# Kernel tuning notes

Hardware: AMD Instinct MI355X
Metric: run time of the kernel (lower is better)

Reference implementation:

```python
import jax, jax.numpy as jnp
import numpy as np

N, M, H, C = 20000, 20000, 32, 128
KP_EXTENT = 0.6
EPS = 1e-5


def _kpconv(q_pts, s_pts, neighb_inds, x, kernel_points, weights):
    """Rigid KPConv, linear influence, 'sum' aggregation, Predator-style density norm."""
    # shadow point / shadow feature padding (index M is the shadow slot)
    s_pad = jnp.concatenate([s_pts, jnp.full((1, 3), 1e6, s_pts.dtype)], axis=0)
    x_pad = jnp.concatenate([x, jnp.zeros((1, x.shape[1]), x.dtype)], axis=0)
    neighbors = s_pad[neighb_inds] - q_pts[:, None, :]              # [N,H,3]
    diff = neighbors[:, :, None, :] - kernel_points[None, None]      # [N,H,K,3]
    sq = jnp.sum(diff * diff, axis=-1)                               # [N,H,K]
    dist = jnp.sqrt(jnp.maximum(sq, 1e-12))
    all_weights = jnp.clip(1.0 - dist / KP_EXTENT, 0.0, None)        # linear KP influence
    neighb_x = x_pad[neighb_inds]                                    # [N,H,C]
    weighted = jnp.einsum('nhk,nhc->nkc', all_weights, neighb_x)     # [N,K,C]
    out = jnp.einsum('nkc,kcd->nd', weighted, weights)               # [N,D]
    # density normalization by number of valid neighbors
    feat_sum = jnp.sum(neighb_x, axis=-1)                            # [N,H]
    n_num = jnp.maximum(jnp.sum(feat_sum > 0.0, axis=-1), 1)         # [N]
    return out / n_num[:, None].astype(out.dtype)


def _segment_norm(x, len0):
    """Per-cloud (instance) normalization over stacked points, 2 clouds, no affine."""
    n = x.shape[0]
    seg = (jnp.arange(n) >= len0).astype(jnp.int32)                  # [N] in {0,1}
    onehot = jax.nn.one_hot(seg, 2, dtype=x.dtype)                   # [N,2]
    cnt = jnp.maximum(onehot.sum(axis=0), 1.0)                       # [2]
    mean = (onehot.T @ x) / cnt[:, None]                             # [2,C]
    var = (onehot.T @ (x * x)) / cnt[:, None] - mean * mean          # [2,C]
    return (x - mean[seg]) * jax.lax.rsqrt(var[seg] + EPS)


def _batchnorm1d(x, gamma, beta):
    mean = jnp.mean(x, axis=0)
    var = jnp.mean(x * x, axis=0) - mean * mean                      # biased, as torch BN
    return (x - mean) * jax.lax.rsqrt(var + EPS) * gamma + beta


def _rand_kernel_points(key, k, radius):
    pts = jax.random.normal(key, (k, 3), dtype=jnp.float32)
    pts = pts / jnp.linalg.norm(pts, axis=1, keepdims=True)
    r = jax.random.uniform(jax.random.fold_in(key, 1), (k, 1)) ** (1.0 / 3.0)
    return pts * r * radius


def setup_inputs() -> dict:
    key = jax.random.key(0)
    ks = jax.random.split(key, 10)
    D = C // 2  # 64, per-branch out channels
    q_pts = jax.random.uniform(ks[0], (N, 3), dtype=jnp.float32)
    s_pts = jax.random.uniform(ks[1], (M, 3), dtype=jnp.float32)
    neighb_inds = jax.random.randint(ks[2], (N, H), 0, M)
    x = jax.random.normal(ks[3], (M, C), dtype=jnp.float32)
    stack_lengths_post = jnp.array([N // 2, N - N // 2], dtype=jnp.int32)
    kp_mini = _rand_kernel_points(ks[4], 7, 1.0 * 1.5)               # radius * 1.5
    w_mini = jax.random.normal(ks[5], (7, C, D), dtype=jnp.float32) * (1.0 / np.sqrt(C))
    kp_mid = _rand_kernel_points(ks[6], 13, 1.0)                      # radius
    w_mid = jax.random.normal(ks[7], (13, C, D), dtype=jnp.float32) * (1.0 / np.sqrt(C))
    w_midmini = jax.random.normal(ks[8], (D, D), dtype=jnp.float32) * (1.0 / np.sqrt(D))
    w_final = jax.random.normal(ks[9], (C, C), dtype=jnp.float32) * (1.0 / np.sqrt(C))
    gamma_final = jnp.ones((C,), jnp.float32)
    beta_final = jnp.zeros((C,), jnp.float32)
    return dict(q_pts=q_pts, s_pts=s_pts, neighb_inds=neighb_inds, x=x,
                stack_lengths_post=stack_lengths_post,
                kp_mini=kp_mini, w_mini=w_mini, kp_mid=kp_mid, w_mid=w_mid,
                w_midmini=w_midmini, w_final=w_final,
                gamma_final=gamma_final, beta_final=beta_final)


def reference(q_pts, s_pts, neighb_inds, x, stack_lengths_post,
              kp_mini, w_mini, kp_mid, w_mid, w_midmini, w_final,
              gamma_final, beta_final):
    len0 = stack_lengths_post[0]
    x1 = _kpconv(q_pts, s_pts, neighb_inds, x, kp_mini, w_mini)      # [N, C//2]
    x1 = _segment_norm(x1, len0)
    x2 = _kpconv(q_pts, s_pts, neighb_inds, x, kp_mid, w_mid)        # [N, C//2]
    x2 = _segment_norm(x2, len0)
    x2 = (x1 + x2) @ w_midmini.T                                     # nn.Linear(bias=False)
    xc = jnp.concatenate([x1, x2], axis=1)                           # [N, C]
    out = xc @ w_final.T
    out = _batchnorm1d(out, gamma_final, beta_final)
    return jax.nn.relu(out)
```

## Files before the change

### kernel.cpp

```cpp
#include <hip/hip_runtime.h>
#include <math.h>

#define NQ 20000
#define MS 20000
#define HN 32
#define CH 128
#define DH 64
#define KTOT 20
#define KMINI 7
#define EPSN 1e-5f
#define KDIM 2560
#define NKT 80
#define NMT 1250
#define KT_Y1 28

#define OFF_ROWSUM 0
#define OFF_Y1     20480
#define OFF_Y2     (OFF_Y1 + NQ*DH)
#define OFF_SEGSUM (OFF_Y2 + NQ*DH)
#define OFF_BNSUM  (OFF_SEGSUM + 512)
#define OFF_BNSQ   (OFF_BNSUM + 128)
#define OFF_OUTPRE (OFF_BNSQ + 128)
#define OFF_WSWZ   (OFF_OUTPRE + NQ*CH)
#define OFF_CFRAG  (OFF_WSWZ + 163840)
#define OFF_XBF    (OFF_CFRAG + 8192)
#define OFF_P      (OFF_XBF + NQ*CH/2)
#define TOT_FLOATS (OFF_P + NQ*KDIM/2)

typedef __attribute__((ext_vector_type(8))) short bf16x8;
typedef __attribute__((ext_vector_type(4))) float f32x4;
typedef __attribute__((ext_vector_type(2))) float f32x2;
typedef __attribute__((ext_vector_type(4))) unsigned short us4;
typedef __attribute__((ext_vector_type(8))) unsigned short us8;

static __device__ inline unsigned short f2bf(float f) {
    unsigned int u = __float_as_uint(f);
    unsigned int r = (u + 0x7fffu + ((u >> 16) & 1u)) >> 16;
    return (unsigned short)r;
}

__global__ __launch_bounds__(256) void k_prep(
    const float* __restrict__ x, float* __restrict__ rowsum,
    const float* __restrict__ w_mini, const float* __restrict__ w_mid,
    const float* __restrict__ w_midmini, const float* __restrict__ w_final,
    unsigned short* __restrict__ wswz, unsigned short* __restrict__ cfrag,
    unsigned short* __restrict__ x_bf)
{
    const int t = threadIdx.x;
    if (blockIdx.x < 1250) {
        int row = blockIdx.x * 16 + (t >> 4);
        int l16 = t & 15;
        const float4* xr = (const float4*)&x[(size_t)row * CH + l16 * 8];
        float4 a = xr[0], b = xr[1];
        if (x_bf) {
            us8 v;
            v[0] = f2bf(a.x); v[1] = f2bf(a.y); v[2] = f2bf(a.z); v[3] = f2bf(a.w);
            v[4] = f2bf(b.x); v[5] = f2bf(b.y); v[6] = f2bf(b.z); v[7] = f2bf(b.w);
            *(us8*)&x_bf[(size_t)row * CH + l16 * 8] = v;
        }
        double s = (double)a.x + a.y + a.z + a.w + b.x + b.y + b.z + b.w;
        #pragma unroll
        for (int off = 8; off > 0; off >>= 1) s += __shfl_down(s, off, 64);
        if (l16 == 0) rowsum[row] = (float)s;
    } else if (blockIdx.x < 2530) {
        int gid = (blockIdx.x - 1250) * 256 + t;
        if (gid >= NKT * 8 * 512) return;
        int j = gid & 7;
        int l = (gid >> 3) & 63;
        int ntkt = gid >> 9;
        int nt = ntkt & 7;
        int kt = ntkt >> 3;
        int kg = kt * 32 + ((l >> 4) << 3) + j;
        int d  = nt * 16 + (l & 15);
        int k = kg >> 7, c = kg & 127;
        float v = 0.0f;
        if (k < KMINI && d < DH)        v = w_mini[((size_t)k * CH + c) * DH + d];
        else if (k >= KMINI && d >= DH) v = w_mid[((size_t)(k - KMINI) * CH + c) * DH + (d - DH)];
        wswz[gid] = f2bf(v);
    } else {
        int b2 = blockIdx.x - 2530;
        int kt = b2 >> 3, nt = b2 & 7;
        for (int e = t; e < 512; e += 256) {
            int l = e >> 3, j = e & 7;
            int i = kt * 32 + ((l >> 4) << 3) + j;
            int jcol = nt * 16 + (l & 15);
            const float* wfr = &w_final[(size_t)jcol * 128 + 64];
            int ec = i & 63;
            float dsum = 0.f;
            #pragma unroll 8
            for (int dd = 0; dd < 64; ++dd)
                dsum += w_midmini[dd * 64 + ec] * wfr[dd];
            float cv = dsum + ((i < 64) ? w_final[(size_t)jcol * 128 + i] : 0.f);
            cfrag[(size_t)(kt * 8 + nt) * 512 + e] = f2bf(cv);
        }
    }
}

__global__ __launch_bounds__(256) void k_gather(
    const float* __restrict__ q_pts, const float* __restrict__ s_pts,
    const int* __restrict__ inds, const unsigned short* __restrict__ x_bf,
    const float* __restrict__ kp_mini, const float* __restrict__ kp_mid,
    const float* __restrict__ rowsum,
    unsigned short* __restrict__ P)
{
    __shared__ __align__(16) float kpts[KTOT][3];
    __shared__ __align__(16) float nb[256][3];
    __shared__ int   nidx[256];
    __shared__ int   vcnt[8];
    __shared__ float winv[8];
    __shared__ __align__(16) float wts[8][HN][KTOT];

    const int t = threadIdx.x;
    const int n0 = blockIdx.x * 8;

    if (t < KTOT * 3) {
        int k = t / 3, j = t % 3;
        kpts[k][j] = (k < KMINI) ? kp_mini[k * 3 + j] : kp_mid[(k - KMINI) * 3 + j];
    }
    if (t < 8) vcnt[t] = 0;
    __syncthreads();

    {
        int r = t >> 5, h = t & 31;
        int n = n0 + r;
        int idx = inds[n * HN + h];
        nidx[t] = idx;
        float qx = q_pts[n * 3 + 0], qy = q_pts[n * 3 + 1], qz = q_pts[n * 3 + 2];
        nb[t][0] = s_pts[idx * 3 + 0] - qx;
        nb[t][1] = s_pts[idx * 3 + 1] - qy;
        nb[t][2] = s_pts[idx * 3 + 2] - qz;
        if (rowsum[idx] > 0.0f) atomicAdd(&vcnt[r], 1);
    }
    __syncthreads();
    if (t < 8) winv[t] = 1.0f / (float)max(vcnt[t], 1);
    __syncthreads();

    for (int tt = t; tt < 8 * HN * KTOT; tt += 256) {
        int r = tt / (HN * KTOT);
        int rem = tt % (HN * KTOT);
        int h = rem / KTOT, k = rem % KTOT;
        float dx = nb[r * HN + h][0] - kpts[k][0];
        float dy = nb[r * HN + h][1] - kpts[k][1];
        float dz = nb[r * HN + h][2] - kpts[k][2];
        float sq = dx * dx + dy * dy + dz * dz;
        float dist = sqrtf(fmaxf(sq, 1e-12f));
        float w = fmaxf(1.0f - dist * (1.0f / 0.6f), 0.0f);
        wts[r][h][k] = w * winv[r];
    }
    __syncthreads();

    const int r = t >> 5;
    const int c4 = t & 31;
    f32x2 acc[KTOT][2];
    #pragma unroll
    for (int k = 0; k < KTOT; ++k) {
        acc[k][0] = (f32x2){0.f, 0.f};
        acc[k][1] = (f32x2){0.f, 0.f};
    }
    const float* wbase = &wts[r][0][0];
    const int* nid = &nidx[r * HN];
    #pragma unroll 2
    for (int h = 0; h < HN; ++h) {
        int idx = nid[h];
        const unsigned int* xp = (const unsigned int*)&x_bf[(size_t)idx * CH + c4 * 4];
        unsigned int u0 = xp[0], u1 = xp[1];
        f32x2 xlo, xhi;
        xlo[0] = __uint_as_float(u0 << 16);
        xlo[1] = __uint_as_float(u0 & 0xffff0000u);
        xhi[0] = __uint_as_float(u1 << 16);
        xhi[1] = __uint_as_float(u1 & 0xffff0000u);
        const float4* wp = (const float4*)(wbase + h * KTOT);
        float warr[20];
        *(float4*)&warr[0]  = wp[0];
        *(float4*)&warr[4]  = wp[1];
        *(float4*)&warr[8]  = wp[2];
        *(float4*)&warr[12] = wp[3];
        *(float4*)&warr[16] = wp[4];
        #pragma unroll
        for (int k = 0; k < KTOT; ++k) {
            float wv = warr[k];
            acc[k][0] += wv * xlo;
            acc[k][1] += wv * xhi;
        }
    }
    const int n = n0 + r;
    const int mt = n >> 4, m15 = n & 15;
    const int lq = (c4 & 7) >> 1;
    const int l = lq * 16 + m15;
    const int j = (c4 & 1) * 4;
    #pragma unroll
    for (int k = 0; k < KTOT; ++k) {
        int kt = k * 4 + (c4 >> 3);
        us4 v;
        v[0] = f2bf(acc[k][0][0]); v[1] = f2bf(acc[k][0][1]);
        v[2] = f2bf(acc[k][1][0]); v[3] = f2bf(acc[k][1][1]);
        *(us4*)(P + ((size_t)mt * NKT + kt) * 512 + l * 8 + j) = v;
    }
}

__global__ __launch_bounds__(256) void k_mfma(
    const unsigned short* __restrict__ P, const unsigned short* __restrict__ wswz,
    const int* __restrict__ stacklen,
    float* __restrict__ y1, float* __restrict__ y2, float* __restrict__ segsum)
{
    const int t = threadIdx.x;
    const int l = t & 63;
    const int w = t >> 6;
    const int chunk = blockIdx.y;
    const int mtb = blockIdx.x * 8 + w * 2;
    if (mtb >= NMT) return;
    const int kb = chunk ? KT_Y1 : 0;
    const int ke = chunk ? NKT : KT_Y1;
    const int ntb = chunk ? 4 : 0;

    f32x4 acc[2][4];
    #pragma unroll
    for (int i = 0; i < 2; ++i)
        #pragma unroll
        for (int q = 0; q < 4; ++q) acc[i][q] = (f32x4){0.f, 0.f, 0.f, 0.f};

    const size_t astride = (size_t)NKT * 512;
    const unsigned short* a0p = P + (size_t)mtb * astride + l * 8;
    const unsigned short* a1p = (mtb + 1 < NMT) ? a0p + astride : a0p;
    const unsigned short* bp = wswz + l * 8;

    #pragma unroll 2
    for (int kt = kb; kt < ke; ++kt) {
        bf16x8 a0 = *(const bf16x8*)(a0p + (size_t)kt * 512);
        bf16x8 a1 = *(const bf16x8*)(a1p + (size_t)kt * 512);
        #pragma unroll
        for (int q = 0; q < 4; ++q) {
            bf16x8 b = *(const bf16x8*)(bp + (size_t)((kt * 8) + ntb + q) * 512);
            acc[0][q] = __builtin_amdgcn_mfma_f32_16x16x32_bf16(a0, b, acc[0][q], 0, 0, 0);
            acc[1][q] = __builtin_amdgcn_mfma_f32_16x16x32_bf16(a1, b, acc[1][q], 0, 0, 0);
        }
    }

    const int len0 = stacklen[0];
    float* yb = chunk ? y2 : y1;
    const int quad = l >> 4, c16 = l & 15;
    const int base_sum = (chunk * 2) * 2 * 64;

    #pragma unroll
    for (int i = 0; i < 2; ++i) {
        int mt = mtb + i;
        if (mt >= NMT) break;
        bool all0 = (mt * 16 + 15 < len0);
        bool all1 = (mt * 16 >= len0);
        #pragma unroll
        for (int q = 0; q < 4; ++q) {
            float s0 = 0.f, q0 = 0.f, s1 = 0.f, q1 = 0.f;
            #pragma unroll
            for (int reg = 0; reg < 4; ++reg) {
                int row = mt * 16 + quad * 4 + reg;
                float v = acc[i][q][reg];
                yb[(size_t)row * DH + q * 16 + c16] = v;
                if (row < len0) { s0 += v; q0 += v * v; }
                else            { s1 += v; q1 += v * v; }
            }
            s0 += __shfl_xor(s0, 16); s0 += __shfl_xor(s0, 32);
            q0 += __shfl_xor(q0, 16); q0 += __shfl_xor(q0, 32);
            s1 += __shfl_xor(s1, 16); s1 += __shfl_xor(s1, 32);
            q1 += __shfl_xor(q1, 16); q1 += __shfl_xor(q1, 32);
            if (quad == 0) {
                int ch = q * 16 + c16;
                if (!all1) {
                    atomicAdd(&segsum[base_sum + 0 * 64 + ch], s0);
                    atomicAdd(&segsum[base_sum + 1 * 64 + ch], q0);
                }
                if (!all0) {
                    atomicAdd(&segsum[base_sum + 2 * 64 + ch], s1);
                    atomicAdd(&segsum[base_sum + 3 * 64 + ch], q1);
                }
            }
        }
    }
}

__global__ __launch_bounds__(256) void k_tailmm(
    const float* __restrict__ y1, const float* __restrict__ y2,
    const float* __restrict__ segsum, const int* __restrict__ stacklen,
    const unsigned short* __restrict__ cfrag,
    float* __restrict__ outpre, float* __restrict__ bnsum, float* __restrict__ bnsq)
{
    __shared__ __align__(16) unsigned short alds[64 * 136];
    __shared__ float sstat[4][2][64];
    const int t = threadIdx.x;
    const int mb = blockIdx.x * 64;
    const int len0 = stacklen[0];

    {
        int combo = t >> 6, ch = t & 63;
        float cnt = (float)max((combo & 1) ? (NQ - len0) : len0, 1);
        float S = segsum[(combo * 2 + 0) * 64 + ch];
        float Q = segsum[(combo * 2 + 1) * 64 + ch];
        float mean = S / cnt;
        float var = Q / cnt - mean * mean;
        sstat[combo][0][ch] = mean;
        sstat[combo][1][ch] = rsqrtf(fmaxf(var, 0.f) + EPSN);
    }
    __syncthreads();

    for (int tt = t; tt < 64 * 32; tt += 256) {
        int r = tt >> 5, c4 = tt & 31;
        int n = mb + r;
        us4 v4 = (us4){0, 0, 0, 0};
        if (n < NQ) {
            int s = (n >= len0) ? 1 : 0;
            int c = c4 * 4;
            if (c < 64) {
                float4 yv = *(const float4*)&y1[(size_t)n * DH + c];
                v4[0] = f2bf((yv.x - sstat[s][0][c + 0]) * sstat[s][1][c + 0]);
                v4[1] = f2bf((yv.y - sstat[s][0][c + 1]) * sstat[s][1][c + 1]);
                v4[2] = f2bf((yv.z - sstat[s][0][c + 2]) * sstat[s][1][c + 2]);
                v4[3] = f2bf((yv.w - sstat[s][0][c + 3]) * sstat[s][1][c + 3]);
            } else {
                int c2 = c - 64;
                float4 yv = *(const float4*)&y2[(size_t)n * DH + c2];
                v4[0] = f2bf((yv.x - sstat[2 + s][0][c2 + 0]) * sstat[2 + s][1][c2 + 0]);
                v4[1] = f2bf((yv.y - sstat[2 + s][0][c2 + 1]) * sstat[2 + s][1][c2 + 1]);
                v4[2] = f2bf((yv.z - sstat[2 + s][0][c2 + 2]) * sstat[2 + s][1][c2 + 2]);
                v4[3] = f2bf((yv.w - sstat[2 + s][0][c2 + 3]) * sstat[2 + s][1][c2 + 3]);
            }
        }
        *(us4*)(alds + r * 136 + c4 * 4) = v4;
    }
    __syncthreads();

    const int l = t & 63, w = t >> 6;
    f32x4 acc[8];
    #pragma unroll
    for (int q = 0; q < 8; ++q) acc[q] = (f32x4){0.f, 0.f, 0.f, 0.f};

    const unsigned short* ap = alds + (w * 16 + (l & 15)) * 136 + ((l >> 4) << 3);
    const unsigned short* bp = cfrag + l * 8;
    #pragma unroll
    for (int kt = 0; kt < 4; ++kt) {
        bf16x8 a = *(const bf16x8*)(ap + kt * 32);
        #pragma unroll
        for (int nt = 0; nt < 8; ++nt) {
            bf16x8 b = *(const bf16x8*)(bp + (size_t)((kt * 8 + nt) << 9));
            acc[nt] = __builtin_amdgcn_mfma_f32_16x16x32_bf16(a, b, acc[nt], 0, 0, 0);
        }
    }

    const int quad = l >> 4, c16 = l & 15;
    #pragma unroll
    for (int nt = 0; nt < 8; ++nt) {
        float s = 0.f, q = 0.f;
        #pragma unroll
        for (int reg = 0; reg < 4; ++reg) {
            int row = mb + w * 16 + quad * 4 + reg;
            float v = acc[nt][reg];
            if (row < NQ) outpre[(size_t)row * CH + nt * 16 + c16] = v;
            else v = 0.f;
            s += v; q += v * v;
        }
        s += __shfl_xor(s, 16); s += __shfl_xor(s, 32);
        q += __shfl_xor(q, 16); q += __shfl_xor(q, 32);
        if (quad == 0) {
            atomicAdd(&bnsum[nt * 16 + c16], s);
            atomicAdd(&bnsq[nt * 16 + c16], q);
        }
    }
}

__global__ __launch_bounds__(256) void k_kpconv(
    const float* __restrict__ q_pts, const float* __restrict__ s_pts,
    const int* __restrict__ inds, const float* __restrict__ x,
    const float* __restrict__ kp_mini, const float* __restrict__ kp_mid,
    const float* __restrict__ w_mini, const float* __restrict__ w_mid,
    const float* __restrict__ rowsum,
    float* __restrict__ y1, float* __restrict__ y2)
{
    __shared__ __align__(16) float kpts[KTOT][3];
    __shared__ __align__(16) float nb[128][3];
    __shared__ int   nidx[128];
    __shared__ int   vcnt[4];
    __shared__ float winv[4];
    __shared__ __align__(16) float wts[4][HN][KTOT];
    __shared__ __align__(16) float wt[KTOT][CH][4];
    __shared__ __align__(16) float part[128][4];

    const int t = threadIdx.x;
    const int n0 = blockIdx.x * 4;

    if (t < KTOT * 3) {
        int k = t / 3, j = t % 3;
        kpts[k][j] = (k < KMINI) ? kp_mini[k * 3 + j] : kp_mid[(k - KMINI) * 3 + j];
    }
    if (t < 4) vcnt[t] = 0;
    __syncthreads();

    if (t < 128) {
        int r = t >> 5, h = t & 31;
        int n = n0 + r;
        int idx = inds[n * HN + h];
        nidx[t] = idx;
        float qx = q_pts[n * 3 + 0], qy = q_pts[n * 3 + 1], qz = q_pts[n * 3 + 2];
        nb[t][0] = s_pts[idx * 3 + 0] - qx;
        nb[t][1] = s_pts[idx * 3 + 1] - qy;
        nb[t][2] = s_pts[idx * 3 + 2] - qz;
        if (rowsum[idx] > 0.0f) atomicAdd(&vcnt[r], 1);
    }
    __syncthreads();
    if (t < 4) winv[t] = 1.0f / (float)max(vcnt[t], 1);
    __syncthreads();

    for (int tt = t; tt < 4 * HN * KTOT; tt += 256) {
        int r = tt / (HN * KTOT);
        int rem = tt % (HN * KTOT);
        int h = rem / KTOT, k = rem % KTOT;
        float dx = nb[r * HN + h][0] - kpts[k][0];
        float dy = nb[r * HN + h][1] - kpts[k][1];
        float dz = nb[r * HN + h][2] - kpts[k][2];
        float sq = dx * dx + dy * dy + dz * dz;
        float dist = sqrtf(fmaxf(sq, 1e-12f));
        float w = fmaxf(1.0f - dist * (1.0f / 0.6f), 0.0f);
        wts[r][h][k] = w * winv[r];
    }
    __syncthreads();

    {
        const int g = t >> 7;
        const int c = t & 127;
        for (int rr = 0; rr < 2; ++rr) {
            const int r = g + rr * 2;
            float acc[KTOT];
            #pragma unroll
            for (int k = 0; k < KTOT; ++k) acc[k] = 0.0f;
            for (int h = 0; h < HN; ++h) {
                int idx = nidx[r * HN + h];
                float xv = x[(size_t)idx * CH + c];
                const float4* wp = (const float4*)&wts[r][h][0];
                float4 wa = wp[0], wb = wp[1], wc = wp[2], wd = wp[3], we = wp[4];
                acc[0]  += wa.x * xv; acc[1]  += wa.y * xv; acc[2]  += wa.z * xv; acc[3]  += wa.w * xv;
                acc[4]  += wb.x * xv; acc[5]  += wb.y * xv; acc[6]  += wb.z * xv; acc[7]  += wb.w * xv;
                acc[8]  += wc.x * xv; acc[9]  += wc.y * xv; acc[10] += wc.z * xv; acc[11] += wc.w * xv;
                acc[12] += wd.x * xv; acc[13] += wd.y * xv; acc[14] += wd.z * xv; acc[15] += wd.w * xv;
                acc[16] += we.x * xv; acc[17] += we.y * xv; acc[18] += we.z * xv; acc[19] += we.w * xv;
            }
            #pragma unroll
            for (int k = 0; k < KTOT; ++k) wt[k][c][r] = acc[k];
        }
    }
    __syncthreads();

    {
        const int d = t & 127;
        const int half = t >> 7;
        const int c0 = half * 64;
        float o0 = 0.f, o1 = 0.f, o2 = 0.f, o3 = 0.f;
        if (d < DH) {
            for (int k = 0; k < KMINI; ++k) {
                const float* wp = &w_mini[((size_t)k * CH + c0) * DH + d];
                for (int c = c0; c < c0 + 64; ++c) {
                    float wv = *wp; wp += DH;
                    const float4 wtv = *(const float4*)&wt[k][c][0];
                    o0 += wv * wtv.x; o1 += wv * wtv.y; o2 += wv * wtv.z; o3 += wv * wtv.w;
                }
            }
        } else {
            const int dd = d - DH;
            for (int k = KMINI; k < KTOT; ++k) {
                const float* wp = &w_mid[((size_t)(k - KMINI) * CH + c0) * DH + dd];
                for (int c = c0; c < c0 + 64; ++c) {
                    float wv = *wp; wp += DH;
                    const float4 wtv = *(const float4*)&wt[k][c][0];
                    o0 += wv * wtv.x; o1 += wv * wtv.y; o2 += wv * wtv.z; o3 += wv * wtv.w;
                }
            }
        }
        if (half == 1) { part[d][0] = o0; part[d][1] = o1; part[d][2] = o2; part[d][3] = o3; }
        __syncthreads();
        if (half == 0) {
            o0 += part[d][0]; o1 += part[d][1]; o2 += part[d][2]; o3 += part[d][3];
            if (d < DH) {
                y1[(size_t)(n0 + 0) * DH + d] = o0;
                y1[(size_t)(n0 + 1) * DH + d] = o1;
                y1[(size_t)(n0 + 2) * DH + d] = o2;
                y1[(size_t)(n0 + 3) * DH + d] = o3;
            } else {
                const int dd = d - DH;
                y2[(size_t)(n0 + 0) * DH + dd] = o0;
                y2[(size_t)(n0 + 1) * DH + dd] = o1;
                y2[(size_t)(n0 + 2) * DH + dd] = o2;
                y2[(size_t)(n0 + 3) * DH + dd] = o3;
            }
        }
    }
}

__global__ __launch_bounds__(256) void k_segpart(
    const float* __restrict__ y1, const float* __restrict__ y2,
    const int* __restrict__ stacklen, float* __restrict__ segsum)
{
    const int t = threadIdx.x;
    const int ch = t & 63, grp = t >> 6;
    const int len0 = stacklen[0];
    float a0 = 0.f, a1 = 0.f, a2 = 0.f, a3 = 0.f;
    float b0 = 0.f, b1 = 0.f, b2 = 0.f, b3 = 0.f;
    for (int r = blockIdx.x * 4 + grp; r < NQ; r += 256 * 4) {
        float v1 = y1[(size_t)r * DH + ch];
        float v2 = y2[(size_t)r * DH + ch];
        bool in1 = (r >= len0);
        float m0 = in1 ? 0.f : 1.f, m1 = 1.f - m0;
        a0 += m0 * v1; a1 += m0 * v1 * v1; a2 += m1 * v1; a3 += m1 * v1 * v1;
        b0 += m0 * v2; b1 += m0 * v2 * v2; b2 += m1 * v2; b3 += m1 * v2 * v2;
    }
    __shared__ float red[4][8][64];
    red[grp][0][ch] = a0; red[grp][1][ch] = a1; red[grp][2][ch] = a2; red[grp][3][ch] = a3;
    red[grp][4][ch] = b0; red[grp][5][ch] = b1; red[grp][6][ch] = b2; red[grp][7][ch] = b3;
    __syncthreads();
    for (int tt = t; tt < 512; tt += 256) {
        int j = tt >> 6, c = tt & 63;
        float s = red[0][j][c] + red[1][j][c] + red[2][j][c] + red[3][j][c];
        atomicAdd(&segsum[j * 64 + c], s);
    }
}

__global__ __launch_bounds__(256) void k_tail(
    const float* __restrict__ y1, const float* __restrict__ y2,
    const float* __restrict__ segsum, const int* __restrict__ stacklen,
    const float* __restrict__ w_midmini, const float* __restrict__ w_final,
    float* __restrict__ outpre, float* __restrict__ bnsum, float* __restrict__ bnsq)
{
    __shared__ __align__(16) float sstat[4][2][64];
    __shared__ __align__(16) float sbuf[8][64];
    __shared__ __align__(16) float xc[8][128];
    __shared__ float lsum[2][128], lsq[2][128];
    const int n0 = blockIdx.x * 8;
    const int t = threadIdx.x;
    const int len0 = stacklen[0];

    {
        int combo = t >> 6, ch = t & 63;
        float cnt = (float)max((combo & 1) ? (NQ - len0) : len0, 1);
        float S = segsum[(combo * 2 + 0) * 64 + ch];
        float Q = segsum[(combo * 2 + 1) * 64 + ch];
        float mean = S / cnt;
        float var = Q / cnt - mean * mean;
        sstat[combo][0][ch] = mean;
        sstat[combo][1][ch] = rsqrtf(fmaxf(var, 0.f) + EPSN);
    }
    __syncthreads();

    for (int tt = t; tt < 8 * 64; tt += 256) {
        int r = tt >> 6, d = tt & 63;
        int n = n0 + r;
        int s = (n >= len0) ? 1 : 0;
        float x1n = (y1[(size_t)n * DH + d] - sstat[s][0][d]) * sstat[s][1][d];
        float x2n = (y2[(size_t)n * DH + d] - sstat[2 + s][0][d]) * sstat[2 + s][1][d];
        xc[r][d] = x1n;
        sbuf[r][d] = x1n + x2n;
    }
    __syncthreads();

    for (int tt = t; tt < 8 * 64; tt += 256) {
        int r = tt >> 6, d = tt & 63;
        float a = 0.f;
        const float4* wmr = (const float4*)&w_midmini[(size_t)d * 64];
        const float4* sv = (const float4*)&sbuf[r][0];
        #pragma unroll
        for (int e4 = 0; e4 < 16; ++e4) {
            float4 w4 = wmr[e4], s4 = sv[e4];
            a += w4.x * s4.x + w4.y * s4.y + w4.z * s4.z + w4.w * s4.w;
        }
        xc[r][64 + d] = a;
    }
    __syncthreads();

    {
        const int j = t & 127;
        const int g = t >> 7;
        float o0 = 0.f, o1 = 0.f, o2 = 0.f, o3 = 0.f;
        const float4* wfr = (const float4*)&w_final[(size_t)j * 128];
        #pragma unroll 8
        for (int i4 = 0; i4 < 32; ++i4) {
            float4 wf = wfr[i4];
            float4 a0 = *(const float4*)&xc[g + 0][i4 * 4];
            float4 a1 = *(const float4*)&xc[g + 2][i4 * 4];
            float4 a2 = *(const float4*)&xc[g + 4][i4 * 4];
            float4 a3 = *(const float4*)&xc[g + 6][i4 * 4];
            o0 += wf.x * a0.x + wf.y * a0.y + wf.z * a0.z + wf.w * a0.w;
            o1 += wf.x * a1.x + wf.y * a1.y + wf.z * a1.z + wf.w * a1.w;
            o2 += wf.x * a2.x + wf.y * a2.y + wf.z * a2.z + wf.w * a2.w;
            o3 += wf.x * a3.x + wf.y * a3.y + wf.z * a3.z + wf.w * a3.w;
        }
        outpre[(size_t)(n0 + g + 0) * CH + j] = o0;
        outpre[(size_t)(n0 + g + 2) * CH + j] = o1;
        outpre[(size_t)(n0 + g + 4) * CH + j] = o2;
        outpre[(size_t)(n0 + g + 6) * CH + j] = o3;
        lsum[g][j] = o0 + o1 + o2 + o3;
        lsq[g][j]  = o0 * o0 + o1 * o1 + o2 * o2 + o3 * o3;
        __syncthreads();
        if (g == 0) {
            atomicAdd(&bnsum[j], lsum[0][j] + lsum[1][j]);
            atomicAdd(&bnsq[j],  lsq[0][j] + lsq[1][j]);
        }
    }
}

__global__ __launch_bounds__(256) void k_bnapply(const float* __restrict__ outpre,
    const float* __restrict__ bnsum, const float* __restrict__ bnsq,
    const float* __restrict__ gamma, const float* __restrict__ beta,
    float* __restrict__ out)
{
    int e4 = blockIdx.x * 256 + threadIdx.x;
    if (e4 >= NQ * CH / 4) return;
    int j0 = (e4 * 4) & 127;
    float4 v = ((const float4*)outpre)[e4];
    float vv[4] = {v.x, v.y, v.z, v.w};
    float res[4];
    #pragma unroll
    for (int i = 0; i < 4; ++i) {
        int j = j0 + i;
        float mean = bnsum[j] * (1.0f / NQ);
        float var = bnsq[j] * (1.0f / NQ) - mean * mean;
        float rstd = rsqrtf(fmaxf(var, 0.f) + EPSN);
        float r = (vv[i] - mean) * rstd * gamma[j] + beta[j];
        res[i] = fmaxf(r, 0.f);
    }
    ((float4*)out)[e4] = make_float4(res[0], res[1], res[2], res[3]);
}

extern "C" void kernel_launch(void* const* d_in, const int* in_sizes, int n_in,
                              void* d_out, int out_size, void* d_ws, size_t ws_size,
                              hipStream_t stream) {
    const float* q_pts     = (const float*)d_in[0];
    const float* s_pts     = (const float*)d_in[1];
    const int*   inds      = (const int*)d_in[2];
    const float* x         = (const float*)d_in[3];
    const int*   stacklen  = (const int*)d_in[4];
    const float* kp_mini   = (const float*)d_in[5];
    const float* w_mini    = (const float*)d_in[6];
    const float* kp_mid    = (const float*)d_in[7];
    const float* w_mid     = (const float*)d_in[8];
    const float* w_midmini = (const float*)d_in[9];
    const float* w_final   = (const float*)d_in[10];
    const float* gamma     = (const float*)d_in[11];
    const float* beta      = (const float*)d_in[12];

    float* ws      = (float*)d_ws;
    float* rowsum  = ws + OFF_ROWSUM;
    float* y1      = ws + OFF_Y1;
    float* y2      = ws + OFF_Y2;
    float* segsum  = ws + OFF_SEGSUM;
    float* bnsum   = ws + OFF_BNSUM;
    float* bnsq    = ws + OFF_BNSQ;
    float* outpre  = ws + OFF_OUTPRE;
    unsigned short* wswz  = (unsigned short*)(ws + OFF_WSWZ);
    unsigned short* cfrag = (unsigned short*)(ws + OFF_CFRAG);
    unsigned short* x_bf  = (unsigned short*)(ws + OFF_XBF);
    unsigned short* P     = (unsigned short*)(ws + OFF_P);

    hipMemsetAsync(segsum, 0, 768 * sizeof(float), stream);

    if (ws_size >= (size_t)TOT_FLOATS * sizeof(float)) {
        k_prep<<<1250 + 1280 + 32, 256, 0, stream>>>(x, rowsum, w_mini, w_mid,
                                                     w_midmini, w_final, wswz, cfrag, x_bf);
        k_gather<<<NQ / 8, 256, 0, stream>>>(q_pts, s_pts, inds, x_bf, kp_mini, kp_mid,
                                             rowsum, P);
        dim3 mg((NMT + 7) / 8, 2);
        k_mfma<<<mg, 256, 0, stream>>>(P, wswz, stacklen, y1, y2, segsum);
        k_tailmm<<<(NQ + 63) / 64, 256, 0, stream>>>(y1, y2, segsum, stacklen, cfrag,
                                                     outpre, bnsum, bnsq);
    } else {
        k_prep<<<1250, 256, 0, stream>>>(x, rowsum, w_mini, w_mid,
                                         w_midmini, w_final, wswz, cfrag, (unsigned short*)0);
        k_kpconv<<<NQ / 4, 256, 0, stream>>>(q_pts, s_pts, inds, x, kp_mini, kp_mid,
                                             w_mini, w_mid, rowsum, y1, y2);
        k_segpart<<<256, 256, 0, stream>>>(y1, y2, stacklen, segsum);
        k_tail<<<NQ / 8, 256, 0, stream>>>(y1, y2, segsum, stacklen, w_midmini, w_final,
                                           outpre, bnsum, bnsq);
    }

    k_bnapply<<<(NQ * CH / 4 + 255) / 256, 256, 0, stream>>>(outpre, bnsum, bnsq,
                                                             gamma, beta, (float*)d_out);
}
```

Measured before the change: 271.4 us.

## Compute per-point kernel-weighted neighbor aggregation with bf16 MFMA instead of FMA

The gather kernel now stores the kernel-point influence weights as bf16 in a transposed shared tile, and stages each point's gathered neighbor features transposed in shared memory. It then computes the [K,H]x[H,C] product with 16x16x32 bf16 MFMA instructions instead of per-thread scalar FMA accumulation. This removes the large register accumulator array and the FP32 FMA work, but adds bf16 rounding of the weights, scattered 2-byte stores into P, and wasted MFMA lanes for K padded from 20 to 32.

Result: slower. 280.0 us (+3.2%).

```diff
diff --git a/kernel.cpp b/kernel.cpp
--- a/kernel.cpp
+++ b/kernel.cpp
@@ -29,7 +29,6 @@
 
 typedef __attribute__((ext_vector_type(8))) short bf16x8;
 typedef __attribute__((ext_vector_type(4))) float f32x4;
-typedef __attribute__((ext_vector_type(2))) float f32x2;
 typedef __attribute__((ext_vector_type(4))) unsigned short us4;
 typedef __attribute__((ext_vector_type(8))) unsigned short us8;
 
@@ -96,22 +95,27 @@
     }
 }
 
-__global__ __launch_bounds__(256) void k_gather(
+__global__ __launch_bounds__(256) void k_wgt(
     const float* __restrict__ q_pts, const float* __restrict__ s_pts,
     const int* __restrict__ inds, const unsigned short* __restrict__ x_bf,
     const float* __restrict__ kp_mini, const float* __restrict__ kp_mid,
     const float* __restrict__ rowsum,
     unsigned short* __restrict__ P)
 {
-    __shared__ __align__(16) float kpts[KTOT][3];
+    __shared__ __align__(16) unsigned short wts_t[8][32][40];
+    __shared__ __align__(16) unsigned short XgT[4][128 * 40];
     __shared__ __align__(16) float nb[256][3];
     __shared__ int   nidx[256];
+    __shared__ float kpts[KTOT][3];
     __shared__ int   vcnt[8];
     __shared__ float winv[8];
-    __shared__ __align__(16) float wts[8][HN][KTOT];
 
     const int t = threadIdx.x;
+    const int l = t & 63;
+    const int w = t >> 6;
     const int n0 = blockIdx.x * 8;
+    const int c16 = l & 15;
+    const int quad = l >> 4;
 
     if (t < KTOT * 3) {
         int k = t / 3, j = t % 3;
@@ -135,66 +139,64 @@
     if (t < 8) winv[t] = 1.0f / (float)max(vcnt[t], 1);
     __syncthreads();
 
-    for (int tt = t; tt < 8 * HN * KTOT; tt += 256) {
-        int r = tt / (HN * KTOT);
-        int rem = tt % (HN * KTOT);
-        int h = rem / KTOT, k = rem % KTOT;
-        float dx = nb[r * HN + h][0] - kpts[k][0];
-        float dy = nb[r * HN + h][1] - kpts[k][1];
-        float dz = nb[r * HN + h][2] - kpts[k][2];
-        float sq = dx * dx + dy * dy + dz * dz;
-        float dist = sqrtf(fmaxf(sq, 1e-12f));
-        float w = fmaxf(1.0f - dist * (1.0f / 0.6f), 0.0f);
-        wts[r][h][k] = w * winv[r];
-    }
-    __syncthreads();
-
-    const int r = t >> 5;
-    const int c4 = t & 31;
-    f32x2 acc[KTOT][2];
-    #pragma unroll
-    for (int k = 0; k < KTOT; ++k) {
-        acc[k][0] = (f32x2){0.f, 0.f};
-        acc[k][1] = (f32x2){0.f, 0.f};
-    }
-    const float* wbase = &wts[r][0][0];
-    const int* nid = &nidx[r * HN];
-    #pragma unroll 2
-    for (int h = 0; h < HN; ++h) {
-        int idx = nid[h];
-        const unsigned int* xp = (const unsigned int*)&x_bf[(size_t)idx * CH + c4 * 4];
-        unsigned int u0 = xp[0], u1 = xp[1];
-        f32x2 xlo, xhi;
-        xlo[0] = __uint_as_float(u0 << 16);
-        xlo[1] = __uint_as_float(u0 & 0xffff0000u);
-        xhi[0] = __uint_as_float(u1 << 16);
-        xhi[1] = __uint_as_float(u1 & 0xffff0000u);
-        const float4* wp = (const float4*)(wbase + h * KTOT);
-        float warr[20];
-        *(float4*)&warr[0]  = wp[0];
-        *(float4*)&warr[4]  = wp[1];
-        *(float4*)&warr[8]  = wp[2];
-        *(float4*)&warr[12] = wp[3];
-        *(float4*)&warr[16] = wp[4];
-        #pragma unroll
-        for (int k = 0; k < KTOT; ++k) {
-            float wv = warr[k];
-            acc[k][0] += wv * xlo;
-            acc[k][1] += wv * xhi;
-        }
-    }
-    const int n = n0 + r;
-    const int mt = n >> 4, m15 = n & 15;
-    const int lq = (c4 & 7) >> 1;
-    const int l = lq * 16 + m15;
-    const int j = (c4 & 1) * 4;
-    #pragma unroll
-    for (int k = 0; k < KTOT; ++k) {
-        int kt = k * 4 + (c4 >> 3);
-        us4 v;
-        v[0] = f2bf(acc[k][0][0]); v[1] = f2bf(acc[k][0][1]);
-        v[2] = f2bf(acc[k][1][0]); v[3] = f2bf(acc[k][1][1]);
-        *(us4*)(P + ((size_t)mt * NKT + kt) * 512 + l * 8 + j) = v;
+    for (int tt = t; tt < 8 * 32 * 32; tt += 256) {
+        int r = tt >> 10;
+        int k = (tt >> 5) & 31;
+        int h = tt & 31;
+        float v = 0.f;
+        if (k < KTOT) {
+            float dx = nb[r * HN + h][0] - kpts[k][0];
+            float dy = nb[r * HN + h][1] - kpts[k][1];
+            float dz = nb[r * HN + h][2] - kpts[k][2];
+            float sq = dx * dx + dy * dy + dz * dz;
+            float dist = sqrtf(fmaxf(sq, 1e-12f));
+            v = fmaxf(1.0f - dist * (1.0f / 0.6f), 0.0f) * winv[r];
+        }
+        wts_t[r][k][h] = f2bf(v);
+    }
+    __syncthreads();
+
+    unsigned short* xt = &XgT[w][0];
+    for (int step = 0; step < 2; ++step) {
+        const int qi = w * 2 + step;
+        const int n = n0 + qi;
+        #pragma unroll
+        for (int i = 0; i < 8; ++i) {
+            int id = i * 64 + l;
+            int h = id & 31, cg = id >> 5;
+            int idx = nidx[qi * HN + h];
+            us8 v = *(const us8*)&x_bf[(size_t)idx * CH + cg * 8];
+            #pragma unroll
+            for (int e = 0; e < 8; ++e)
+                xt[(cg * 8 + e) * 40 + h] = v[e];
+        }
+        bf16x8 a0 = *(const bf16x8*)&wts_t[qi][c16][quad * 8];
+        bf16x8 a1 = *(const bf16x8*)&wts_t[qi][16 + c16][quad * 8];
+        const int mt = n >> 4, n15 = n & 15;
+        unsigned short* pbase = P + (size_t)mt * NKT * 512;
+        #pragma unroll
+        for (int nt = 0; nt < 8; ++nt) {
+            bf16x8 b = *(const bf16x8*)&xt[(nt * 16 + c16) * 40 + quad * 8];
+            f32x4 d0 = __builtin_amdgcn_mfma_f32_16x16x32_bf16(a0, b, (f32x4){0.f,0.f,0.f,0.f}, 0, 0, 0);
+            f32x4 d1 = __builtin_amdgcn_mfma_f32_16x16x32_bf16(a1, b, (f32x4){0.f,0.f,0.f,0.f}, 0, 0, 0);
+            const int c = nt * 16 + c16;
+            const int lq = (c & 31) >> 3;
+            const int jj = c & 7;
+            const int ktc = c >> 5;
+            const size_t off = (size_t)lq * 16 * 8 + (size_t)n15 * 8 + jj;
+            #pragma unroll
+            for (int reg = 0; reg < 4; ++reg) {
+                int k0 = quad * 4 + reg;
+                pbase[(size_t)(k0 * 4 + ktc) * 512 + off] = f2bf(d0[reg]);
+            }
+            if (quad == 0) {
+                #pragma unroll
+                for (int reg = 0; reg < 4; ++reg) {
+                    int k1 = 16 + reg;
+                    pbase[(size_t)(k1 * 4 + ktc) * 512 + off] = f2bf(d1[reg]);
+                }
+            }
+        }
     }
 }
 
@@ -659,8 +661,8 @@
     if (ws_size >= (size_t)TOT_FLOATS * sizeof(float)) {
         k_prep<<<1250 + 1280 + 32, 256, 0, stream>>>(x, rowsum, w_mini, w_mid,
                                                      w_midmini, w_final, wswz, cfrag, x_bf);
-        k_gather<<<NQ / 8, 256, 0, stream>>>(q_pts, s_pts, inds, x_bf, kp_mini, kp_mid,
-                                             rowsum, P);
+        k_wgt<<<NQ / 8, 256, 0, stream>>>(q_pts, s_pts, inds, x_bf, kp_mini, kp_mid,
+                                          rowsum, P);
         dim3 mg((NMT + 7) / 8, 2);
         k_mfma<<<mg, 256, 0, stream>>>(P, wswz, stacklen, y1, y2, segsum);
         k_tailmm<<<(NQ + 63) / 64, 256, 0, stream>>>(y1, y2, segsum, stacklen, cfrag,
```
